# Performance work log

Measured on AMD Instinct MI355X. Metric: run time of the kernel, lower is better.

## Reference

```python
import jax, jax.numpy as jnp
import numpy as np

EPS = 1e-12
ATTEND_SCALE = 8.0

def _l2norm(t, axis=-1):
    n = jnp.sqrt(jnp.sum(t * t, axis=axis, keepdims=True))
    return t / jnp.maximum(n, EPS)

def setup_inputs() -> dict:
    key = jax.random.key(0)
    k1, k2, k3, k4 = jax.random.split(key, 4)
    b, n, dim = 4, 8192, 1024
    heads, dim_head = 16, 64
    dim_inner = heads * dim_head
    x = jax.random.normal(k1, (b, n, dim), dtype=jnp.float32)
    gamma = jnp.ones((dim,), dtype=jnp.float32)  # RMSNorm gamma
    # torch Linear(dim, 3*dim_inner, bias=False): store as [dim, 3*dim_inner] for x @ W
    w_qkv = jax.random.normal(k2, (dim, 3 * dim_inner), dtype=jnp.float32) * (dim ** -0.5)
    temperature = jnp.zeros((heads, 1, 1), dtype=jnp.float32)
    w_out = jax.random.normal(k3, (dim_inner, dim), dtype=jnp.float32) * (dim_inner ** -0.5)
    return {"x": x, "gamma": gamma, "w_qkv": w_qkv, "temperature": temperature, "w_out": w_out}

def reference(x, gamma, w_qkv, temperature, w_out):
    b, n, dim = x.shape
    heads = temperature.shape[0]
    dim_head = w_qkv.shape[1] // (3 * heads)
    # RMSNorm: F.normalize(x, dim=-1) * sqrt(dim) * gamma
    xn = _l2norm(x) * (dim ** 0.5) * gamma
    qkv = xn @ w_qkv  # [b, n, 3*h*d]
    qkv = qkv.reshape(b, n, 3, heads, dim_head).transpose(2, 0, 3, 4, 1)  # [3, b, h, d, n]
    q, k, v = qkv[0], qkv[1], qkv[2]
    orig_v = v
    # l2-normalize q, k over the sequence axis (last dim of [b,h,d,n])
    q = _l2norm(q) * jnp.exp(temperature)  # temperature [h,1,1] broadcasts
    k = _l2norm(k)
    # attention over the feature axis: sim [b, h, d, d]
    sim = jnp.einsum('bhdn,bhen->bhde', q, k) * ATTEND_SCALE
    attn = jax.nn.softmax(sim, axis=-1)
    out = jnp.einsum('bhde,bhen->bhdn', attn, v)  # [b, h, d, n]
    out = out.transpose(0, 3, 1, 2).reshape(b, n, heads * dim_head) @ w_out  # [b, n, dim]
    return out, orig_v
```

## Files before the change

kernel.cpp:

```cpp
#include <hip/hip_runtime.h>
#include <hip/hip_bf16.h>

#define DEVI __device__ __forceinline__

using bf16x8 = __attribute__((ext_vector_type(8))) __bf16;
using f32x4  = __attribute__((ext_vector_type(4))) float;
using u16x8  = __attribute__((ext_vector_type(8))) unsigned short;

DEVI unsigned short f2bf(float f) {
  unsigned int u = __float_as_uint(f);
  u = (u + 0x7FFFu + ((u >> 16) & 1u)) >> 16;
  return (unsigned short)u;
}
DEVI float bf2f(unsigned short s) { return __uint_as_float(((unsigned int)s) << 16); }

DEVI void gld_lds16(const unsigned short* g, unsigned short* l) {
  __builtin_amdgcn_global_load_lds(
      (const __attribute__((address_space(1))) void*)g,
      (__attribute__((address_space(3))) void*)l, 16, 0, 0);
}

__global__ __launch_bounds__(256) void transpose_cast_kernel(const float* __restrict__ in,
                                                             unsigned short* __restrict__ out,
                                                             int R, int C) {
  __shared__ float tile[32][33];
  const int c0 = blockIdx.x * 32, r0 = blockIdx.y * 32;
  const int tx = threadIdx.x & 31, ty = threadIdx.x >> 5;
  for (int rr = ty; rr < 32; rr += 8)
    tile[rr][tx] = in[(size_t)(r0 + rr) * C + c0 + tx];
  __syncthreads();
  for (int cc = ty; cc < 32; cc += 8)
    out[(size_t)(c0 + cc) * R + r0 + tx] = f2bf(tile[tx][cc]);
}

__global__ __launch_bounds__(256) void transpose_bf16_kernel(const unsigned short* __restrict__ in,
                                                             unsigned short* __restrict__ out,
                                                             int R, int C) {
  __shared__ unsigned short tile[32][33];
  const int c0 = blockIdx.x * 32, r0 = blockIdx.y * 32;
  const int tx = threadIdx.x & 31, ty = threadIdx.x >> 5;
  for (int rr = ty; rr < 32; rr += 8)
    tile[rr][tx] = in[(size_t)(r0 + rr) * C + c0 + tx];
  __syncthreads();
  for (int cc = ty; cc < 32; cc += 8)
    out[(size_t)(c0 + cc) * R + r0 + tx] = tile[tx][cc];
}

__global__ __launch_bounds__(256) void rmsnorm_kernel(const float* __restrict__ x,
                                                      const float* __restrict__ gamma,
                                                      unsigned short* __restrict__ xn) {
  __shared__ float wsum[4];
  const int row = blockIdx.x;
  const int t = threadIdx.x;
  const float4 v = *(const float4*)&x[(size_t)row * 1024 + t * 4];
  float s = v.x * v.x + v.y * v.y + v.z * v.z + v.w * v.w;
  for (int off = 32; off; off >>= 1) s += __shfl_down(s, off);
  if ((t & 63) == 0) wsum[t >> 6] = s;
  __syncthreads();
  const float tot = wsum[0] + wsum[1] + wsum[2] + wsum[3];
  const float scale = 32.0f / fmaxf(sqrtf(tot), 1e-12f);
  const float4 g = *(const float4*)&gamma[t * 4];
  ushort4 o;
  o.x = f2bf(v.x * scale * g.x);
  o.y = f2bf(v.y * scale * g.y);
  o.z = f2bf(v.z * scale * g.z);
  o.w = f2bf(v.w * scale * g.w);
  *(ushort4*)&xn[(size_t)row * 1024 + t * 4] = o;
}

__global__ __launch_bounds__(256) void gemm_gram_kernel(const unsigned short* __restrict__ xnT,
                                                        unsigned short* __restrict__ Gp) {
  if (blockIdx.x > blockIdx.y) return;
  __shared__ __align__(16) unsigned short Al[4096];
  __shared__ __align__(16) unsigned short Bl[4096];
  const int tid = threadIdx.x;
  const int lane = tid & 63, wid = tid >> 6;
  const int wr = wid >> 1, wc = wid & 1;
  const int r = lane & 15, kg = lane >> 4;
  const int rw0 = tid >> 2, q0 = (tid & 3) * 8;
  const size_t row0 = (size_t)blockIdx.y * 128, col0 = (size_t)blockIdx.x * 128;
  const int z = blockIdx.z;
  const size_t koff = (size_t)(z >> 2) * 8192 + (size_t)(z & 3) * 2048;
  f32x4 acc[4][4] = {};
  for (int k0 = 0; k0 < 2048; k0 += 32) {
    __syncthreads();
    gld_lds16(&xnT[(row0 + rw0) * 32768 + koff + k0 + q0], &Al[tid * 8]);
    gld_lds16(&xnT[(row0 + rw0 + 64) * 32768 + koff + k0 + q0], &Al[2048 + tid * 8]);
    gld_lds16(&xnT[(col0 + rw0) * 32768 + koff + k0 + q0], &Bl[tid * 8]);
    gld_lds16(&xnT[(col0 + rw0 + 64) * 32768 + koff + k0 + q0], &Bl[2048 + tid * 8]);
    __syncthreads();
    bf16x8 af[4], bfr[4];
#pragma unroll
    for (int m = 0; m < 4; ++m) af[m] = *(const bf16x8*)&Al[(wr * 64 + m * 16 + r) * 32 + kg * 8];
#pragma unroll
    for (int n = 0; n < 4; ++n) bfr[n] = *(const bf16x8*)&Bl[(wc * 64 + n * 16 + r) * 32 + kg * 8];
#pragma unroll
    for (int m = 0; m < 4; ++m)
#pragma unroll
      for (int n = 0; n < 4; ++n)
        acc[m][n] = __builtin_amdgcn_mfma_f32_16x16x32_bf16(af[m], bfr[n], acc[m][n], 0, 0, 0);
  }
  unsigned short* C = Gp + ((size_t)z << 20);
  const int rbase = wr * 64 + (lane >> 4) * 4;
  const int cbase = wc * 64 + (lane & 15);
#pragma unroll
  for (int m = 0; m < 4; ++m)
#pragma unroll
    for (int n = 0; n < 4; ++n)
#pragma unroll
      for (int j = 0; j < 4; ++j)
        C[(row0 + rbase + m * 16 + j) * 1024 + col0 + cbase + n * 16] = f2bf(acc[m][n][j]);
}

__global__ __launch_bounds__(256) void greduce_kernel(const unsigned short* __restrict__ Gp,
                                                      unsigned short* __restrict__ G) {
  const int tj = blockIdx.x, ti = blockIdx.y, b = blockIdx.z;
  if ((tj >> 1) > (ti >> 1)) return;
  __shared__ float lds[64][65];
  const int t = threadIdx.x;
  const int r = t >> 2, c0 = (t & 3) * 16;
  const size_t idx = (size_t)(ti * 64 + r) * 1024 + tj * 64 + c0;
  float v[16];
#pragma unroll
  for (int j = 0; j < 16; ++j) v[j] = 0.f;
  for (int s = 0; s < 4; ++s) {
    const unsigned short* p = Gp + ((size_t)(b * 4 + s) << 20) + idx;
#pragma unroll
    for (int j = 0; j < 16; ++j) v[j] += bf2f(p[j]);
  }
  unsigned short* Gb = G + ((size_t)b << 20);
  __attribute__((aligned(16))) unsigned short buf[16];
#pragma unroll
  for (int j = 0; j < 16; ++j) buf[j] = f2bf(v[j]);
  { int4* dst = (int4*)&Gb[idx]; const int4* src = (const int4*)buf; dst[0] = src[0]; dst[1] = src[1]; }
  if ((ti >> 1) != (tj >> 1)) {
#pragma unroll
    for (int j = 0; j < 16; ++j) lds[r][c0 + j] = v[j];
    __syncthreads();
    const int x = t >> 2, y0 = (t & 3) * 16;
#pragma unroll
    for (int j = 0; j < 16; ++j) buf[j] = f2bf(lds[y0 + j][x]);
    int4* dst = (int4*)&Gb[(size_t)(tj * 64 + x) * 1024 + ti * 64 + y0];
    const int4* src = (const int4*)buf;
    dst[0] = src[0]; dst[1] = src[1];
  }
}

__global__ __launch_bounds__(256) void gemm_bt_batch_bf16(const unsigned short* __restrict__ A,
                                                          const unsigned short* __restrict__ Bt,
                                                          unsigned short* __restrict__ C,
                                                          int N, int K,
                                                          long long aStr, long long bStr, long long cStr) {
  __shared__ __align__(16) unsigned short Al[4096];
  __shared__ __align__(16) unsigned short Bl[4096];
  A += (size_t)blockIdx.z * aStr; Bt += (size_t)blockIdx.z * bStr; C += (size_t)blockIdx.z * cStr;
  const int tid = threadIdx.x;
  const int lane = tid & 63, wid = tid >> 6;
  const int wr = wid >> 1, wc = wid & 1;
  const int r = lane & 15, kg = lane >> 4;
  const int rw0 = tid >> 2, q0 = (tid & 3) * 8;
  const size_t row0 = (size_t)blockIdx.y * 128, col0 = (size_t)blockIdx.x * 128;
  f32x4 acc[4][4] = {};
  for (int k0 = 0; k0 < K; k0 += 32) {
    __syncthreads();
    gld_lds16(&A[(row0 + rw0) * K + k0 + q0], &Al[tid * 8]);
    gld_lds16(&A[(row0 + rw0 + 64) * K + k0 + q0], &Al[2048 + tid * 8]);
    gld_lds16(&Bt[(col0 + rw0) * K + k0 + q0], &Bl[tid * 8]);
    gld_lds16(&Bt[(col0 + rw0 + 64) * K + k0 + q0], &Bl[2048 + tid * 8]);
    __syncthreads();
    bf16x8 af[4], bfr[4];
#pragma unroll
    for (int m = 0; m < 4; ++m) af[m] = *(const bf16x8*)&Al[(wr * 64 + m * 16 + r) * 32 + kg * 8];
#pragma unroll
    for (int n = 0; n < 4; ++n) bfr[n] = *(const bf16x8*)&Bl[(wc * 64 + n * 16 + r) * 32 + kg * 8];
#pragma unroll
    for (int m = 0; m < 4; ++m)
#pragma unroll
      for (int n = 0; n < 4; ++n)
        acc[m][n] = __builtin_amdgcn_mfma_f32_16x16x32_bf16(af[m], bfr[n], acc[m][n], 0, 0, 0);
  }
  const int rbase = wr * 64 + (lane >> 4) * 4;
  const int cbase = wc * 64 + (lane & 15);
#pragma unroll
  for (int m = 0; m < 4; ++m)
#pragma unroll
    for (int n = 0; n < 4; ++n)
#pragma unroll
      for (int j = 0; j < 4; ++j)
        C[(row0 + rbase + m * 16 + j) * N + col0 + cbase + n * 16] = f2bf(acc[m][n][j]);
}

__global__ __launch_bounds__(256) void gemm_bt_batch_f32(const unsigned short* __restrict__ A,
                                                         const unsigned short* __restrict__ Bt,
                                                         float* __restrict__ C,
                                                         int N, int K,
                                                         long long aStr, long long bStr, long long cStr) {
  __shared__ __align__(16) unsigned short Al[4096];
  __shared__ __align__(16) unsigned short Bl[4096];
  A += (size_t)blockIdx.z * aStr; Bt += (size_t)blockIdx.z * bStr; C += (size_t)blockIdx.z * cStr;
  const int tid = threadIdx.x;
  const int lane = tid & 63, wid = tid >> 6;
  const int wr = wid >> 1, wc = wid & 1;
  const int r = lane & 15, kg = lane >> 4;
  const int rw0 = tid >> 2, q0 = (tid & 3) * 8;
  const size_t row0 = (size_t)blockIdx.y * 128, col0 = (size_t)blockIdx.x * 128;
  f32x4 acc[4][4] = {};
  for (int k0 = 0; k0 < K; k0 += 32) {
    __syncthreads();
    gld_lds16(&A[(row0 + rw0) * K + k0 + q0], &Al[tid * 8]);
    gld_lds16(&A[(row0 + rw0 + 64) * K + k0 + q0], &Al[2048 + tid * 8]);
    gld_lds16(&Bt[(col0 + rw0) * K + k0 + q0], &Bl[tid * 8]);
    gld_lds16(&Bt[(col0 + rw0 + 64) * K + k0 + q0], &Bl[2048 + tid * 8]);
    __syncthreads();
    bf16x8 af[4], bfr[4];
#pragma unroll
    for (int m = 0; m < 4; ++m) af[m] = *(const bf16x8*)&Al[(wr * 64 + m * 16 + r) * 32 + kg * 8];
#pragma unroll
    for (int n = 0; n < 4; ++n) bfr[n] = *(const bf16x8*)&Bl[(wc * 64 + n * 16 + r) * 32 + kg * 8];
#pragma unroll
    for (int m = 0; m < 4; ++m)
#pragma unroll
      for (int n = 0; n < 4; ++n)
        acc[m][n] = __builtin_amdgcn_mfma_f32_16x16x32_bf16(af[m], bfr[n], acc[m][n], 0, 0, 0);
  }
  const int rbase = wr * 64 + (lane >> 4) * 4;
  const int cbase = wc * 64 + (lane & 15);
#pragma unroll
  for (int m = 0; m < 4; ++m)
#pragma unroll
    for (int n = 0; n < 4; ++n)
#pragma unroll
      for (int j = 0; j < 4; ++j)
        C[(row0 + rbase + m * 16 + j) * N + col0 + cbase + n * 16] = acc[m][n][j];
}

__global__ __launch_bounds__(256) void gemm_v_kernel(const unsigned short* __restrict__ A,
                                                     const unsigned short* __restrict__ BtV,
                                                     unsigned short* __restrict__ vbn,
                                                     float* __restrict__ origv) {
  __shared__ __align__(16) unsigned short Al[4096];
  __shared__ __align__(16) unsigned short Bl[4096];
  const int tid = threadIdx.x;
  const int lane = tid & 63, wid = tid >> 6;
  const int wr = wid >> 1, wc = wid & 1;
  const int r = lane & 15, kg = lane >> 4;
  const int rw0 = tid >> 2, q0 = (tid & 3) * 8;
  const size_t row0 = (size_t)blockIdx.y * 128, col0 = (size_t)blockIdx.x * 128;
  const int K = 1024;
  f32x4 acc[4][4] = {};
  for (int k0 = 0; k0 < K; k0 += 32) {
    __syncthreads();
    gld_lds16(&A[(row0 + rw0) * K + k0 + q0], &Al[tid * 8]);
    gld_lds16(&A[(row0 + rw0 + 64) * K + k0 + q0], &Al[2048 + tid * 8]);
    gld_lds16(&BtV[(col0 + rw0) * K + k0 + q0], &Bl[tid * 8]);
    gld_lds16(&BtV[(col0 + rw0 + 64) * K + k0 + q0], &Bl[2048 + tid * 8]);
    __syncthreads();
    bf16x8 af[4], bfr[4];
#pragma unroll
    for (int m = 0; m < 4; ++m) af[m] = *(const bf16x8*)&Al[(wr * 64 + m * 16 + r) * 32 + kg * 8];
#pragma unroll
    for (int n = 0; n < 4; ++n) bfr[n] = *(const bf16x8*)&Bl[(wc * 64 + n * 16 + r) * 32 + kg * 8];
#pragma unroll
    for (int m = 0; m < 4; ++m)
#pragma unroll
      for (int n = 0; n < 4; ++n)
        acc[m][n] = __builtin_amdgcn_mfma_f32_16x16x32_bf16(af[m], bfr[n], acc[m][n], 0, 0, 0);
  }
  const int rbase = wr * 64 + (lane >> 4) * 4;
  const int cbase = wc * 64 + (lane & 15);
  const int b = (int)(row0 >> 13);
  const int nn0 = (int)(row0 & 8191) + rbase;
#pragma unroll
  for (int m = 0; m < 4; ++m)
#pragma unroll
    for (int n = 0; n < 4; ++n) {
      const int hd = (int)col0 + cbase + n * 16;
      float4 o4;
      o4.x = acc[m][n][0]; o4.y = acc[m][n][1]; o4.z = acc[m][n][2]; o4.w = acc[m][n][3];
      *(float4*)&origv[((size_t)b * 1024 + hd) * 8192 + nn0 + m * 16] = o4;
#pragma unroll
      for (int j = 0; j < 4; ++j)
        vbn[(row0 + rbase + m * 16 + j) * 1024 + hd] = f2bf(acc[m][n][j]);
    }
}

__global__ __launch_bounds__(256) void sim_softmax_kernel(const unsigned short* __restrict__ wqkvT,
                                                          const unsigned short* __restrict__ UTt,
                                                          const float* __restrict__ temperature,
                                                          float* __restrict__ attn) {
  __shared__ __align__(16) unsigned short Aql[64 * 128];
  __shared__ __align__(16) unsigned short Bkl[64 * 128];
  __shared__ float qknl[2][64];
  const int bh = blockIdx.x;
  const int b = bh >> 4, h = bh & 15;
  const int t = threadIdx.x;
  const int lane = t & 63, w = t >> 6;
  const unsigned short* UTtb = UTt + ((size_t)b << 21);
  if (t < 128) {
    const int sel = t >> 6, dd = t & 63;
    const size_t roff = (size_t)(sel * 1024 + h * 64 + dd) * 1024;
    const unsigned short* pa = UTtb + roff;
    const unsigned short* pb = wqkvT + roff;
    float nv = 0.f;
    for (int i = 0; i < 1024; i += 8) {
      const u16x8 va = *(const u16x8*)&pa[i];
      const u16x8 vb = *(const u16x8*)&pb[i];
#pragma unroll
      for (int j = 0; j < 8; ++j) nv += bf2f(va[j]) * bf2f(vb[j]);
    }
    qknl[sel][dd] = fmaxf(sqrtf(nv), 1e-12f);
  }
  const unsigned short* AqG = UTtb + (size_t)(h * 64) * 1024;
  const unsigned short* BkG = wqkvT + (size_t)(1024 + h * 64) * 1024;
  const int r = lane & 15, kg = lane >> 4;
  const int srow = t >> 4, scol = (t & 15) * 8;
  f32x4 acc[4] = {};
  for (int k0 = 0; k0 < 1024; k0 += 128) {
    __syncthreads();
#pragma unroll
    for (int c = 0; c < 4; ++c) {
      gld_lds16(&AqG[(size_t)(c * 16 + srow) * 1024 + k0 + scol], &Aql[c * 2048 + t * 8]);
      gld_lds16(&BkG[(size_t)(c * 16 + srow) * 1024 + k0 + scol], &Bkl[c * 2048 + t * 8]);
    }
    __syncthreads();
#pragma unroll
    for (int kk = 0; kk < 128; kk += 32) {
      const bf16x8 af = *(const bf16x8*)&Aql[(w * 16 + r) * 128 + kk + kg * 8];
#pragma unroll
      for (int n = 0; n < 4; ++n) {
        const bf16x8 bfr = *(const bf16x8*)&Bkl[(n * 16 + r) * 128 + kk + kg * 8];
        acc[n] = __builtin_amdgcn_mfma_f32_16x16x32_bf16(af, bfr, acc[n], 0, 0, 0);
      }
    }
  }
  const float sc = 8.f * __expf(temperature[h]);
  const int colq = lane & 15, rq = lane >> 4;
#pragma unroll
  for (int j = 0; j < 4; ++j) {
    const int d = w * 16 + rq * 4 + j;
    const float qd = qknl[0][d];
    float sv[4];
#pragma unroll
    for (int n = 0; n < 4; ++n) sv[n] = acc[n][j] * sc / (qd * qknl[1][n * 16 + colq]);
    float mj = fmaxf(fmaxf(sv[0], sv[1]), fmaxf(sv[2], sv[3]));
    for (int msk = 1; msk < 16; msk <<= 1) mj = fmaxf(mj, __shfl_xor(mj, msk));
    float p[4], sum = 0.f;
#pragma unroll
    for (int n = 0; n < 4; ++n) { p[n] = __expf(sv[n] - mj); sum += p[n]; }
    for (int msk = 1; msk < 16; msk <<= 1) sum += __shfl_xor(sum, msk);
    const float inv = 1.f / sum;
#pragma unroll
    for (int n = 0; n < 4; ++n)
      attn[(size_t)bh * 4096 + d * 64 + n * 16 + colq] = p[n] * inv;
  }
}

__global__ __launch_bounds__(256) void w2t_kernel(const float* __restrict__ attn,
                                                  const float* __restrict__ w_out,
                                                  unsigned short* __restrict__ W2T) {
  __shared__ float al[64][64];
  __shared__ float wl[64][64];
  const int bh = blockIdx.y;
  const int b = bh >> 4, h = bh & 15;
  const int c0 = blockIdx.x * 256;
  const int t = threadIdx.x, e = t & 63, g = t >> 6;
  const int dr = t >> 2, q4 = (t & 3) * 16;
#pragma unroll
  for (int j = 0; j < 16; j += 4)
    *(float4*)&al[dr][q4 + j] = *(const float4*)&attn[(size_t)bh * 4096 + dr * 64 + q4 + j];
  for (int cb = 0; cb < 4; ++cb) {
    __syncthreads();
#pragma unroll
    for (int j = 0; j < 16; j += 4)
      *(float4*)&wl[dr][q4 + j] = *(const float4*)&w_out[(size_t)(h * 64 + dr) * 1024 + c0 + cb * 64 + q4 + j];
    __syncthreads();
#pragma unroll
    for (int i = 0; i < 16; ++i) {
      const int cc = g * 16 + i;
      float s = 0.f;
#pragma unroll 8
      for (int d = 0; d < 64; ++d) s += al[d][e] * wl[d][cc];
      W2T[((size_t)b << 20) + (size_t)(c0 + cb * 64 + cc) * 1024 + h * 64 + e] = f2bf(s);
    }
  }
}

extern "C" void kernel_launch(void* const* d_in, const int* in_sizes, int n_in,
                              void* d_out, int out_size, void* d_ws, size_t ws_size,
                              hipStream_t stream) {
  const float* x     = (const float*)d_in[0];
  const float* gamma = (const float*)d_in[1];
  const float* w_qkv = (const float*)d_in[2];
  const float* temp  = (const float*)d_in[3];
  const float* w_out = (const float*)d_in[4];
  char* ws = (char*)d_ws;
  unsigned short* wqkvT = (unsigned short*)(ws);
  unsigned short* xn    = (unsigned short*)(ws + 6291456);
  unsigned short* xnT   = (unsigned short*)(ws + 73400320);
  unsigned short* vbn   = xnT;
  unsigned short* Gp    = (unsigned short*)(ws + 140509184);
  unsigned short* G     = (unsigned short*)(ws + 174063616);
  unsigned short* UTt   = (unsigned short*)(ws + 182452224);
  float* attn           = (float*)(ws + 199229440);
  unsigned short* W2T   = (unsigned short*)(ws + 200278016);
  float* outp  = (float*)d_out;
  float* origv = outp + (size_t)33554432;

  transpose_cast_kernel<<<dim3(96, 32), 256, 0, stream>>>(w_qkv, wqkvT, 1024, 3072);
  rmsnorm_kernel<<<32768, 256, 0, stream>>>(x, gamma, xn);
  transpose_bf16_kernel<<<dim3(32, 1024), 256, 0, stream>>>(xn, xnT, 32768, 1024);
  gemm_gram_kernel<<<dim3(8, 8, 16), 256, 0, stream>>>(xnT, Gp);
  greduce_kernel<<<dim3(16, 16, 4), 256, 0, stream>>>(Gp, G);
  gemm_bt_batch_bf16<<<dim3(8, 16, 4), 256, 0, stream>>>(wqkvT, G, UTt, 1024, 1024,
                                                         0LL, 1LL << 20, 1LL << 21);
  gemm_v_kernel<<<dim3(8, 256), 256, 0, stream>>>(xn, wqkvT + (size_t)2048 * 1024, vbn, origv);
  sim_softmax_kernel<<<64, 256, 0, stream>>>(wqkvT, UTt, temp, attn);
  w2t_kernel<<<dim3(4, 64), 256, 0, stream>>>(attn, w_out, W2T);
  gemm_bt_batch_f32<<<dim3(8, 64, 4), 256, 0, stream>>>(vbn, W2T, outp, 1024, 1024,
                                                        8388608LL, 1LL << 20, 8388608LL);
}
```

Baseline: 567.9 us.

## Fold Wv into per-batch output weights and fuse V and output GEMMs

Instead of materialising bf16 V and then multiplying by W2T, the output projection weights are pre-folded with Wv (WfoldT = W2T·Wv per batch), so out = xn·WfoldT is computed directly from xn. A single combined kernel computes both orig_v tiles and out tiles from the same xn A operand, with a swizzled block order for L2 reuse of xn. The q/k norm reduction moves out of the 64-block sim_softmax kernel into a separate, more parallel norms kernel. This removes the vbn write and read round-trip and a dependent GEMM. It adds a small batched fold GEMM and a cast kernel, and rounds the folded weights to bf16 once more.

```diff
diff --git a/kernel.cpp b/kernel.cpp
--- a/kernel.cpp
+++ b/kernel.cpp
@@ -31,6 +31,16 @@
   __syncthreads();
   for (int cc = ty; cc < 32; cc += 8)
     out[(size_t)(c0 + cc) * R + r0 + tx] = f2bf(tile[tx][cc]);
+}
+
+__global__ __launch_bounds__(256) void castv_kernel(const float* __restrict__ w_qkv,
+                                                    unsigned short* __restrict__ Wv_nt) {
+  const int i = blockIdx.x * 256 + threadIdx.x;
+  const int k = i >> 8, he4 = (i & 255) * 4;
+  const float4 v = *(const float4*)&w_qkv[(size_t)k * 3072 + 2048 + he4];
+  ushort4 o;
+  o.x = f2bf(v.x); o.y = f2bf(v.y); o.z = f2bf(v.z); o.w = f2bf(v.w);
+  *(ushort4*)&Wv_nt[(size_t)k * 1024 + he4] = o;
 }
 
 __global__ __launch_bounds__(256) void transpose_bf16_kernel(const unsigned short* __restrict__ in,
@@ -190,70 +200,34 @@
         C[(row0 + rbase + m * 16 + j) * N + col0 + cbase + n * 16] = f2bf(acc[m][n][j]);
 }
 
-__global__ __launch_bounds__(256) void gemm_bt_batch_f32(const unsigned short* __restrict__ A,
-                                                         const unsigned short* __restrict__ Bt,
-                                                         float* __restrict__ C,
-                                                         int N, int K,
-                                                         long long aStr, long long bStr, long long cStr) {
+__global__ __launch_bounds__(256) void gemm_vout_kernel(const unsigned short* __restrict__ A,
+                                                        const unsigned short* __restrict__ BtV,
+                                                        const unsigned short* __restrict__ WfoldT,
+                                                        float* __restrict__ origv,
+                                                        float* __restrict__ outp) {
   __shared__ __align__(16) unsigned short Al[4096];
   __shared__ __align__(16) unsigned short Bl[4096];
-  A += (size_t)blockIdx.z * aStr; Bt += (size_t)blockIdx.z * bStr; C += (size_t)blockIdx.z * cStr;
+  const int flat = blockIdx.x;
+  const int s = (flat & 7) * 512 + (flat >> 3);
+  const int cb = s & 15, rb = s >> 4;
+  const size_t row0 = (size_t)rb * 128;
+  const int b = rb >> 6;
+  const unsigned short* Bt = (cb < 8)
+      ? BtV + (size_t)cb * 128 * 1024
+      : WfoldT + ((size_t)b << 20) + (size_t)(cb - 8) * 128 * 1024;
   const int tid = threadIdx.x;
   const int lane = tid & 63, wid = tid >> 6;
   const int wr = wid >> 1, wc = wid & 1;
   const int r = lane & 15, kg = lane >> 4;
   const int rw0 = tid >> 2, q0 = (tid & 3) * 8;
-  const size_t row0 = (size_t)blockIdx.y * 128, col0 = (size_t)blockIdx.x * 128;
-  f32x4 acc[4][4] = {};
-  for (int k0 = 0; k0 < K; k0 += 32) {
-    __syncthreads();
-    gld_lds16(&A[(row0 + rw0) * K + k0 + q0], &Al[tid * 8]);
-    gld_lds16(&A[(row0 + rw0 + 64) * K + k0 + q0], &Al[2048 + tid * 8]);
-    gld_lds16(&Bt[(col0 + rw0) * K + k0 + q0], &Bl[tid * 8]);
-    gld_lds16(&Bt[(col0 + rw0 + 64) * K + k0 + q0], &Bl[2048 + tid * 8]);
-    __syncthreads();
-    bf16x8 af[4], bfr[4];
-#pragma unroll
-    for (int m = 0; m < 4; ++m) af[m] = *(const bf16x8*)&Al[(wr * 64 + m * 16 + r) * 32 + kg * 8];
-#pragma unroll
-    for (int n = 0; n < 4; ++n) bfr[n] = *(const bf16x8*)&Bl[(wc * 64 + n * 16 + r) * 32 + kg * 8];
-#pragma unroll
-    for (int m = 0; m < 4; ++m)
-#pragma unroll
-      for (int n = 0; n < 4; ++n)
-        acc[m][n] = __builtin_amdgcn_mfma_f32_16x16x32_bf16(af[m], bfr[n], acc[m][n], 0, 0, 0);
-  }
-  const int rbase = wr * 64 + (lane >> 4) * 4;
-  const int cbase = wc * 64 + (lane & 15);
-#pragma unroll
-  for (int m = 0; m < 4; ++m)
-#pragma unroll
-    for (int n = 0; n < 4; ++n)
-#pragma unroll
-      for (int j = 0; j < 4; ++j)
-        C[(row0 + rbase + m * 16 + j) * N + col0 + cbase + n * 16] = acc[m][n][j];
-}
-
-__global__ __launch_bounds__(256) void gemm_v_kernel(const unsigned short* __restrict__ A,
-                                                     const unsigned short* __restrict__ BtV,
-                                                     unsigned short* __restrict__ vbn,
-                                                     float* __restrict__ origv) {
-  __shared__ __align__(16) unsigned short Al[4096];
-  __shared__ __align__(16) unsigned short Bl[4096];
-  const int tid = threadIdx.x;
-  const int lane = tid & 63, wid = tid >> 6;
-  const int wr = wid >> 1, wc = wid & 1;
-  const int r = lane & 15, kg = lane >> 4;
-  const int rw0 = tid >> 2, q0 = (tid & 3) * 8;
-  const size_t row0 = (size_t)blockIdx.y * 128, col0 = (size_t)blockIdx.x * 128;
   const int K = 1024;
   f32x4 acc[4][4] = {};
   for (int k0 = 0; k0 < K; k0 += 32) {
     __syncthreads();
     gld_lds16(&A[(row0 + rw0) * K + k0 + q0], &Al[tid * 8]);
     gld_lds16(&A[(row0 + rw0 + 64) * K + k0 + q0], &Al[2048 + tid * 8]);
-    gld_lds16(&BtV[(col0 + rw0) * K + k0 + q0], &Bl[tid * 8]);
-    gld_lds16(&BtV[(col0 + rw0 + 64) * K + k0 + q0], &Bl[2048 + tid * 8]);
+    gld_lds16(&Bt[(size_t)rw0 * K + k0 + q0], &Bl[tid * 8]);
+    gld_lds16(&Bt[(size_t)(rw0 + 64) * K + k0 + q0], &Bl[2048 + tid * 8]);
     __syncthreads();
     bf16x8 af[4], bfr[4];
 #pragma unroll
@@ -268,24 +242,52 @@
   }
   const int rbase = wr * 64 + (lane >> 4) * 4;
   const int cbase = wc * 64 + (lane & 15);
-  const int b = (int)(row0 >> 13);
-  const int nn0 = (int)(row0 & 8191) + rbase;
-#pragma unroll
-  for (int m = 0; m < 4; ++m)
-#pragma unroll
-    for (int n = 0; n < 4; ++n) {
-      const int hd = (int)col0 + cbase + n * 16;
-      float4 o4;
-      o4.x = acc[m][n][0]; o4.y = acc[m][n][1]; o4.z = acc[m][n][2]; o4.w = acc[m][n][3];
-      *(float4*)&origv[((size_t)b * 1024 + hd) * 8192 + nn0 + m * 16] = o4;
-#pragma unroll
-      for (int j = 0; j < 4; ++j)
-        vbn[(row0 + rbase + m * 16 + j) * 1024 + hd] = f2bf(acc[m][n][j]);
-    }
+  if (cb < 8) {
+    const int nn0 = (int)(row0 & 8191) + rbase;
+#pragma unroll
+    for (int m = 0; m < 4; ++m)
+#pragma unroll
+      for (int n = 0; n < 4; ++n) {
+        const int hd = cb * 128 + cbase + n * 16;
+        float4 o4;
+        o4.x = acc[m][n][0]; o4.y = acc[m][n][1]; o4.z = acc[m][n][2]; o4.w = acc[m][n][3];
+        *(float4*)&origv[((size_t)b * 1024 + hd) * 8192 + nn0 + m * 16] = o4;
+      }
+  } else {
+    const size_t col0 = (size_t)(cb - 8) * 128;
+#pragma unroll
+    for (int m = 0; m < 4; ++m)
+#pragma unroll
+      for (int n = 0; n < 4; ++n)
+#pragma unroll
+        for (int j = 0; j < 4; ++j)
+          outp[(row0 + rbase + m * 16 + j) * 1024 + col0 + cbase + n * 16] = acc[m][n][j];
+  }
+}
+
+__global__ __launch_bounds__(256) void norms_kernel(const unsigned short* __restrict__ UTt,
+                                                    const unsigned short* __restrict__ wqkvT,
+                                                    float* __restrict__ qkn2) {
+  const int t = threadIdx.x;
+  const int rloc = t >> 4, lane16 = t & 15;
+  const int row = blockIdx.x * 16 + rloc;
+  const int b = row >> 11, r2 = row & 2047;
+  const unsigned short* pa = UTt + ((size_t)b << 21) + (size_t)r2 * 1024 + lane16 * 64;
+  const unsigned short* pb = wqkvT + (size_t)r2 * 1024 + lane16 * 64;
+  float s = 0.f;
+  for (int i = 0; i < 64; i += 8) {
+    const u16x8 va = *(const u16x8*)&pa[i];
+    const u16x8 vb = *(const u16x8*)&pb[i];
+#pragma unroll
+    for (int j = 0; j < 8; ++j) s += bf2f(va[j]) * bf2f(vb[j]);
+  }
+  for (int off = 8; off; off >>= 1) s += __shfl_down(s, off, 16);
+  if (lane16 == 0) qkn2[row] = s;
 }
 
 __global__ __launch_bounds__(256) void sim_softmax_kernel(const unsigned short* __restrict__ wqkvT,
                                                           const unsigned short* __restrict__ UTt,
+                                                          const float* __restrict__ qkn2,
                                                           const float* __restrict__ temperature,
                                                           float* __restrict__ attn) {
   __shared__ __align__(16) unsigned short Aql[64 * 128];
@@ -298,17 +300,7 @@
   const unsigned short* UTtb = UTt + ((size_t)b << 21);
   if (t < 128) {
     const int sel = t >> 6, dd = t & 63;
-    const size_t roff = (size_t)(sel * 1024 + h * 64 + dd) * 1024;
-    const unsigned short* pa = UTtb + roff;
-    const unsigned short* pb = wqkvT + roff;
-    float nv = 0.f;
-    for (int i = 0; i < 1024; i += 8) {
-      const u16x8 va = *(const u16x8*)&pa[i];
-      const u16x8 vb = *(const u16x8*)&pb[i];
-#pragma unroll
-      for (int j = 0; j < 8; ++j) nv += bf2f(va[j]) * bf2f(vb[j]);
-    }
-    qknl[sel][dd] = fmaxf(sqrtf(nv), 1e-12f);
+    qknl[sel][dd] = fmaxf(sqrtf(qkn2[b * 2048 + sel * 1024 + h * 64 + dd]), 1e-12f);
   }
   const unsigned short* AqG = UTtb + (size_t)(h * 64) * 1024;
   const unsigned short* BkG = wqkvT + (size_t)(1024 + h * 64) * 1024;
@@ -394,28 +386,33 @@
   const float* temp  = (const float*)d_in[3];
   const float* w_out = (const float*)d_in[4];
   char* ws = (char*)d_ws;
-  unsigned short* wqkvT = (unsigned short*)(ws);
-  unsigned short* xn    = (unsigned short*)(ws + 6291456);
-  unsigned short* xnT   = (unsigned short*)(ws + 73400320);
-  unsigned short* vbn   = xnT;
-  unsigned short* Gp    = (unsigned short*)(ws + 140509184);
-  unsigned short* G     = (unsigned short*)(ws + 174063616);
-  unsigned short* UTt   = (unsigned short*)(ws + 182452224);
-  float* attn           = (float*)(ws + 199229440);
-  unsigned short* W2T   = (unsigned short*)(ws + 200278016);
+  unsigned short* wqkvT  = (unsigned short*)(ws);
+  unsigned short* Wv_nt  = (unsigned short*)(ws + 6291456);
+  unsigned short* xn     = (unsigned short*)(ws + 8388608);
+  unsigned short* xnT    = (unsigned short*)(ws + 75497472);
+  unsigned short* Gp     = (unsigned short*)(ws + 142606336);
+  unsigned short* G      = (unsigned short*)(ws + 176160768);
+  unsigned short* UTt    = (unsigned short*)(ws + 184549376);
+  float* qkn2            = (float*)(ws + 201326592);
+  float* attn            = (float*)(ws + 201359360);
+  unsigned short* W2T    = (unsigned short*)(ws + 202407936);
+  unsigned short* WfoldT = (unsigned short*)(ws + 210796544);
   float* outp  = (float*)d_out;
   float* origv = outp + (size_t)33554432;
 
   transpose_cast_kernel<<<dim3(96, 32), 256, 0, stream>>>(w_qkv, wqkvT, 1024, 3072);
+  castv_kernel<<<1024, 256, 0, stream>>>(w_qkv, Wv_nt);
   rmsnorm_kernel<<<32768, 256, 0, stream>>>(x, gamma, xn);
   transpose_bf16_kernel<<<dim3(32, 1024), 256, 0, stream>>>(xn, xnT, 32768, 1024);
   gemm_gram_kernel<<<dim3(8, 8, 16), 256, 0, stream>>>(xnT, Gp);
   greduce_kernel<<<dim3(16, 16, 4), 256, 0, stream>>>(Gp, G);
   gemm_bt_batch_bf16<<<dim3(8, 16, 4), 256, 0, stream>>>(wqkvT, G, UTt, 1024, 1024,
                                                          0LL, 1LL << 20, 1LL << 21);
-  gemm_v_kernel<<<dim3(8, 256), 256, 0, stream>>>(xn, wqkvT + (size_t)2048 * 1024, vbn, origv);
-  sim_softmax_kernel<<<64, 256, 0, stream>>>(wqkvT, UTt, temp, attn);
+  norms_kernel<<<512, 256, 0, stream>>>(UTt, wqkvT, qkn2);
+  sim_softmax_kernel<<<64, 256, 0, stream>>>(wqkvT, UTt, qkn2, temp, attn);
   w2t_kernel<<<dim3(4, 64), 256, 0, stream>>>(attn, w_out, W2T);
-  gemm_bt_batch_f32<<<dim3(8, 64, 4), 256, 0, stream>>>(vbn, W2T, outp, 1024, 1024,
-                                                        8388608LL, 1LL << 20, 8388608LL);
-}
+  gemm_bt_batch_bf16<<<dim3(8, 8, 4), 256, 0, stream>>>(W2T, Wv_nt, WfoldT, 1024, 1024,
+                                                        1LL << 20, 0LL, 1LL << 20);
+  gemm_vout_kernel<<<4096, 256, 0, stream>>>(xn, wqkvT + (size_t)2048 * 1024, WfoldT,
+                                             origv, outp);
+}
```

Result: faster. 550.9 us (-3.0%).
